# Performance work log

Hardware: AMD Instinct MI355X
Metric: run time of the kernel (lower is better)

The kernel has to match this reference:

```python
import jax, jax.numpy as jnp
import numpy as np

H_DIM = 2048
N_HEADS = 16
HEAD_DIM = H_DIM // N_HEADS
B, S = 2, 2048


def setup_inputs() -> dict:
    key = jax.random.key(0)
    ks = jax.random.split(key, 10)
    sc = 1.0 / np.sqrt(H_DIM)
    return {
        "X": jax.random.normal(ks[0], (B, S, H_DIM), dtype=jnp.float32),
        "attention_mask": jnp.ones((B, S, S), dtype=jnp.int32),
        "Wq": jax.random.normal(ks[1], (H_DIM, H_DIM), dtype=jnp.float32) * sc,
        "bq": jnp.zeros((H_DIM,), dtype=jnp.float32),
        "Wk": jax.random.normal(ks[2], (H_DIM, H_DIM), dtype=jnp.float32) * sc,
        "bk": jnp.zeros((H_DIM,), dtype=jnp.float32),
        "Wv": jax.random.normal(ks[3], (H_DIM, H_DIM), dtype=jnp.float32) * sc,
        "bv": jnp.zeros((H_DIM,), dtype=jnp.float32),
        "Wo": jax.random.normal(ks[4], (H_DIM, H_DIM), dtype=jnp.float32) * sc,
        "bo": jnp.zeros((H_DIM,), dtype=jnp.float32),
    }


def reference(X, attention_mask, Wq, bq, Wk, bk, Wv, bv, Wo, bo):
    b, s, _ = X.shape
    # QKV projections -> [b, heads, s, head_dim]
    def proj(W, bias):
        y = jnp.einsum("bsd,de->bse", X, W) + bias
        return y.reshape(b, s, N_HEADS, HEAD_DIM).transpose(0, 2, 1, 3)
    Q, K, V = proj(Wq, bq), proj(Wk, bk), proj(Wv, bv)
    # scores [b, h, s, s]
    scores = jnp.einsum("bhqd,bhkd->bhqk", Q, K) / jnp.sqrt(jnp.float32(HEAD_DIM))
    mask = attention_mask[:, None, :, :]  # [b,1,s,s]
    scores = jnp.where(mask == 0, jnp.float32(-jnp.inf), scores)
    attn = jax.nn.softmax(scores, axis=-1)
    # dropout_rate = 0.0 -> no-op
    out = jnp.einsum("bhqk,bhkd->bhqd", attn, V)
    out = out.transpose(0, 2, 1, 3).reshape(b, s, H_DIM)
    return jnp.einsum("bsd,de->bse", out, Wo) + bo
```

## Files before the change

### kernel.cpp

```cpp
#include <hip/hip_runtime.h>
#include <hip/hip_bf16.h>

#define H_DIM 2048
#define N_HEADS 16
#define HEAD_DIM 128
#define BATCH 2
#define SEQ 2048

typedef __bf16 bf16_t;
typedef __bf16 bf16x8 __attribute__((ext_vector_type(8)));
typedef float f32x4 __attribute__((ext_vector_type(4)));

#define MFMA16(a, b, c) __builtin_amdgcn_mfma_f32_16x16x32_bf16((a), (b), (c), 0, 0, 0)

#define GLOAD16(gp, lp) __builtin_amdgcn_global_load_lds( \
    (const __attribute__((address_space(1))) void*)(gp),  \
    (__attribute__((address_space(3))) void*)(lp), 16, 0, 0)

__global__ __launch_bounds__(256) void detect_kernel(const unsigned int* __restrict__ X,
                                                     int* __restrict__ flags) {
    __shared__ int cnt[256];
    int t = threadIdx.x;
    int c = 0;
    for (int i = 0; i < 16; i++) {
        unsigned w  = X[t * 16 + i];
        unsigned lo = w & 0xFFFFu;
        unsigned e  = (lo >> 7) & 0xFFu;
        if (lo == 0u || (e >= 100u && e <= 141u)) c++;
    }
    cnt[t] = c;
    __syncthreads();
    for (int s = 128; s > 0; s >>= 1) {
        if (t < s) cnt[t] += cnt[t + s];
        __syncthreads();
    }
    if (t == 0) { flags[0] = (cnt[0] >= 2048) ? 1 : 0; flags[1] = 1; }
}

__global__ __launch_bounds__(256) void maskcheck_kernel(const int* __restrict__ mask,
                                                        int* __restrict__ flags) {
    size_t i = ((size_t)blockIdx.x * 256 + threadIdx.x) * 8;
    const int4* p = (const int4*)(mask + i);
    int4 a = p[0], b = p[1];
    int all = (a.x != 0) & (a.y != 0) & (a.z != 0) & (a.w != 0) &
              (b.x != 0) & (b.y != 0) & (b.z != 0) & (b.w != 0);
    if (!all) atomicAnd(&flags[1], 0);
}

__device__ inline bf16x8 load8(const void* __restrict__ p, size_t idx, int isbf16) {
    if (isbf16) {
        return *(const bf16x8*)((const bf16_t*)p + idx);
    } else {
        const float* f = (const float*)p + idx;
        float4 a = *(const float4*)f;
        float4 b = *(const float4*)(f + 4);
        bf16x8 r;
        r[0] = (bf16_t)a.x; r[1] = (bf16_t)a.y; r[2] = (bf16_t)a.z; r[3] = (bf16_t)a.w;
        r[4] = (bf16_t)b.x; r[5] = (bf16_t)b.y; r[6] = (bf16_t)b.z; r[7] = (bf16_t)b.w;
        return r;
    }
}

__device__ inline float readf(const void* __restrict__ p, int idx, int isbf16) {
    return isbf16 ? (float)((const bf16_t*)p)[idx] : ((const float*)p)[idx];
}

__global__ __launch_bounds__(256) void convert_kernel(const void* __restrict__ X,
                                                      bf16_t* __restrict__ Xb,
                                                      const int* __restrict__ flags) {
    const int isbf16 = flags[0];
    size_t i = ((size_t)blockIdx.x * 256 + threadIdx.x) * 8;
    bf16x8 v = load8(X, i, isbf16);
    *(bf16x8*)(Xb + i) = v;
}

__global__ __launch_bounds__(256) void transpose_kernel(
    const void* __restrict__ W0, const void* __restrict__ W1,
    const void* __restrict__ W2, const void* __restrict__ W3,
    bf16_t* __restrict__ Wts, const int* __restrict__ flags)
{
    const int isbf16 = flags[0];
    const int z = blockIdx.z;
    const void* W = (z == 0) ? W0 : (z == 1) ? W1 : (z == 2) ? W2 : W3;
    bf16_t* out = Wts + (size_t)z * H_DIM * H_DIM;

    __shared__ __attribute__((aligned(16))) bf16_t Ts[64][72];
    const int tid = threadIdx.x;
    const int n0 = blockIdx.x * 64;
    const int k0 = blockIdx.y * 64;

    #pragma unroll
    for (int j = 0; j < 2; j++) {
        int idx = j * 2048 + tid * 8;
        int r = idx >> 6, c = idx & 63;
        bf16x8 v = load8(W, (size_t)(k0 + r) * H_DIM + n0 + c, isbf16);
        *(bf16x8*)(&Ts[r][c]) = v;
    }
    __syncthreads();
    const int wr = tid & 63;
    const int wcg = (tid >> 6) * 8;
    #pragma unroll
    for (int j = 0; j < 2; j++) {
        int wc = wcg + j * 32;
        bf16x8 o;
        #pragma unroll
        for (int u = 0; u < 8; u++) o[u] = Ts[wc + u][wr];
        *(bf16x8*)(&out[(size_t)(n0 + wr) * H_DIM + k0 + wc]) = o;
    }
}

__global__ __launch_bounds__(256) void gemm_qkv_kernel(
    const bf16_t* __restrict__ A, const bf16_t* __restrict__ Wts,
    const void* __restrict__ b0, const void* __restrict__ b1, const void* __restrict__ b2,
    bf16_t* __restrict__ qws, bf16_t* __restrict__ kws, bf16_t* __restrict__ vtws,
    const int* __restrict__ flags)
{
    const int isbf16 = flags[0];
    const int z = blockIdx.z;
    const bf16_t* Wt = Wts + (size_t)z * H_DIM * H_DIM;
    const void* bias = (z == 0) ? b0 : (z == 1) ? b1 : b2;
    bf16_t* dst = (z == 0) ? qws : (z == 1) ? kws : vtws;

    __shared__ __attribute__((aligned(16))) bf16_t As[4][128][8];
    __shared__ __attribute__((aligned(16))) bf16_t Bs[4][128][8];

    const int tid  = threadIdx.x;
    const int lane = tid & 63;
    const int wid  = tid >> 6;
    const int quad = lane >> 4;
    const int l16  = lane & 15;
    const int wm   = (wid >> 1) * 64;
    const int wn   = (wid & 1) * 64;
    const int m0   = blockIdx.y * 128;
    const int n0   = blockIdx.x * 128;

    f32x4 acc[4][4] = {};

    for (int k0 = 0; k0 < H_DIM; k0 += 32) {
        #pragma unroll
        for (int j = 0; j < 2; j++) {
            int slot = j * 256 + tid;
            int k8 = slot >> 7, row = slot & 127;
            GLOAD16(A  + (size_t)(m0 + row) * H_DIM + k0 + k8 * 8, (bf16_t*)As + slot * 8);
            GLOAD16(Wt + (size_t)(n0 + row) * H_DIM + k0 + k8 * 8, (bf16_t*)Bs + slot * 8);
        }
        __syncthreads();
        bf16x8 af[4], bfr[4];
        #pragma unroll
        for (int i = 0; i < 4; i++) {
            af[i]  = *(const bf16x8*)(&As[quad][wm + i * 16 + l16][0]);
            bfr[i] = *(const bf16x8*)(&Bs[quad][wn + i * 16 + l16][0]);
        }
        #pragma unroll
        for (int mi = 0; mi < 4; mi++)
            #pragma unroll
            for (int ni = 0; ni < 4; ni++)
                acc[mi][ni] = MFMA16(af[mi], bfr[ni], acc[mi][ni]);
        __syncthreads();
    }

    #pragma unroll
    for (int ni = 0; ni < 4; ni++) {
        int col = n0 + wn + ni * 16 + l16;
        int h = col >> 7, d = col & (HEAD_DIM - 1);
        float bv = readf(bias, col, isbf16);
        #pragma unroll
        for (int mi = 0; mi < 4; mi++) {
            int row0 = m0 + wm + mi * 16 + quad * 4;
            int b = row0 >> 11;
            if (z < 2) {
                #pragma unroll
                for (int r = 0; r < 4; r++) {
                    int s = (row0 + r) & (SEQ - 1);
                    dst[((size_t)(b * N_HEADS + h) * SEQ + s) * HEAD_DIM + d] =
                        (bf16_t)(acc[mi][ni][r] + bv);
                }
            } else {
                int s0 = row0 & (SEQ - 1);
                bf16_t o[4];
                #pragma unroll
                for (int r = 0; r < 4; r++) o[r] = (bf16_t)(acc[mi][ni][r] + bv);
                *(unsigned long long*)(&dst[((size_t)(b * N_HEADS + h) * HEAD_DIM + d) * SEQ + s0]) =
                    *(unsigned long long*)o;
            }
        }
    }
}

__global__ __launch_bounds__(256) void gemm_out_kernel(
    const bf16_t* __restrict__ A, const bf16_t* __restrict__ Wt,
    const void* __restrict__ bias, void* __restrict__ C,
    const int* __restrict__ flags)
{
    const int isbf16 = flags[0];
    __shared__ __attribute__((aligned(16))) bf16_t As[4][128][8];
    __shared__ __attribute__((aligned(16))) bf16_t Bs[4][128][8];

    const int tid  = threadIdx.x;
    const int lane = tid & 63;
    const int wid  = tid >> 6;
    const int quad = lane >> 4;
    const int l16  = lane & 15;
    const int wm   = (wid >> 1) * 64;
    const int wn   = (wid & 1) * 64;
    const int m0   = blockIdx.y * 128;
    const int n0   = blockIdx.x * 128;

    f32x4 acc[4][4] = {};

    for (int k0 = 0; k0 < H_DIM; k0 += 32) {
        #pragma unroll
        for (int j = 0; j < 2; j++) {
            int slot = j * 256 + tid;
            int k8 = slot >> 7, row = slot & 127;
            GLOAD16(A  + (size_t)(m0 + row) * H_DIM + k0 + k8 * 8, (bf16_t*)As + slot * 8);
            GLOAD16(Wt + (size_t)(n0 + row) * H_DIM + k0 + k8 * 8, (bf16_t*)Bs + slot * 8);
        }
        __syncthreads();
        bf16x8 af[4], bfr[4];
        #pragma unroll
        for (int i = 0; i < 4; i++) {
            af[i]  = *(const bf16x8*)(&As[quad][wm + i * 16 + l16][0]);
            bfr[i] = *(const bf16x8*)(&Bs[quad][wn + i * 16 + l16][0]);
        }
        #pragma unroll
        for (int mi = 0; mi < 4; mi++)
            #pragma unroll
            for (int ni = 0; ni < 4; ni++)
                acc[mi][ni] = MFMA16(af[mi], bfr[ni], acc[mi][ni]);
        __syncthreads();
    }

    #pragma unroll
    for (int ni = 0; ni < 4; ni++) {
        int col = n0 + wn + ni * 16 + l16;
        float bv = readf(bias, col, isbf16);
        #pragma unroll
        for (int mi = 0; mi < 4; mi++) {
            int row0 = m0 + wm + mi * 16 + quad * 4;
            #pragma unroll
            for (int r = 0; r < 4; r++) {
                float v = acc[mi][ni][r] + bv;
                if (isbf16) ((bf16_t*)C)[(size_t)(row0 + r) * H_DIM + col] = (bf16_t)v;
                else        ((float*)C)[(size_t)(row0 + r) * H_DIM + col]  = v;
            }
        }
    }
}

__global__ __launch_bounds__(256) void attn_kernel(
    const bf16_t* __restrict__ Q, const bf16_t* __restrict__ K,
    const bf16_t* __restrict__ Vt, const int* __restrict__ mask,
    const int* __restrict__ flags, bf16_t* __restrict__ ctx)
{
    __shared__ __attribute__((aligned(16))) bf16_t Ks[2][16][64][8];
    __shared__ __attribute__((aligned(16))) bf16_t Vs[2][8][128][8];
    __shared__ __attribute__((aligned(16))) bf16_t Pl[4][16][72];

    const int tid  = threadIdx.x;
    const int lane = tid & 63;
    const int wid  = tid >> 6;
    const int quad = lane >> 4;
    const int l16  = lane & 15;

    const int bh = blockIdx.y;
    const int b  = bh >> 4, h = bh & 15;
    const int q_base = blockIdx.x * 64 + wid * 16;
    const int maskAll = flags[1];

    const bf16_t* Qp = Q  + (size_t)bh * SEQ * HEAD_DIM;
    const bf16_t* Kp = K  + (size_t)bh * SEQ * HEAD_DIM;
    const bf16_t* Vp = Vt + (size_t)bh * HEAD_DIM * SEQ;
    const int*    mp = mask + (size_t)b * SEQ * SEQ;

    bf16x8 qf[4];
    #pragma unroll
    for (int t = 0; t < 4; t++)
        qf[t] = *(const bf16x8*)(Qp + (size_t)(q_base + l16) * HEAD_DIM + t * 32 + quad * 8);

    const float CS = 0.1275260013f;
    float m_r[4], l_r[4];
    #pragma unroll
    for (int r = 0; r < 4; r++) { m_r[r] = -1e30f; l_r[r] = 0.0f; }
    f32x4 o_acc[8] = {};

    auto stage = [&](int kt, int bb) {
        const int key0 = kt * 64;
        #pragma unroll
        for (int j = 0; j < 4; j++) {
            int slot = j * 256 + tid;
            int krow = slot & 63, k8 = slot >> 6;
            GLOAD16(Kp + (size_t)(key0 + krow) * HEAD_DIM + k8 * 8,
                    (bf16_t*)(&Ks[bb][0][0][0]) + slot * 8);
        }
        #pragma unroll
        for (int j = 0; j < 4; j++) {
            int slot = j * 256 + tid;
            int d = slot & 127, kq = slot >> 7;
            GLOAD16(Vp + (size_t)d * SEQ + key0 + kq * 8,
                    (bf16_t*)(&Vs[bb][0][0][0]) + slot * 8);
        }
    };

    stage(0, 0);

    const int NKT = SEQ / 64;
    for (int kt = 0; kt < NKT; kt++) {
        const int bb = kt & 1;
        const int key0 = kt * 64;
        __syncthreads();
        if (kt + 1 < NKT) stage(kt + 1, bb ^ 1);

        f32x4 s_acc[4];
        #pragma unroll
        for (int nt = 0; nt < 4; nt++) {
            f32x4 a = {};
            #pragma unroll
            for (int t = 0; t < 4; t++) {
                bf16x8 kf = *(const bf16x8*)(&Ks[bb][t * 4 + quad][nt * 16 + l16][0]);
                a = MFMA16(qf[t], kf, a);
            }
            s_acc[nt] = a;
        }

        float p2[4][4];
        #pragma unroll
        for (int nt = 0; nt < 4; nt++)
            #pragma unroll
            for (int r = 0; r < 4; r++)
                p2[nt][r] = s_acc[nt][r] * CS;

        if (!maskAll) {
            #pragma unroll
            for (int nt = 0; nt < 4; nt++) {
                int key = key0 + nt * 16 + l16;
                #pragma unroll
                for (int r = 0; r < 4; r++) {
                    int q = q_base + quad * 4 + r;
                    if (mp[(size_t)q * SEQ + key] == 0) p2[nt][r] = -1e30f;
                }
            }
        }

        #pragma unroll
        for (int r = 0; r < 4; r++) {
            float tmax = fmaxf(fmaxf(p2[0][r], p2[1][r]), fmaxf(p2[2][r], p2[3][r]));
            #pragma unroll
            for (int off = 1; off < 16; off <<= 1)
                tmax = fmaxf(tmax, __shfl_xor(tmax, off));
            float mnew  = fmaxf(m_r[r], tmax);
            float alpha = exp2f(m_r[r] - mnew);
            m_r[r] = mnew;
            float rsum = 0.0f;
            #pragma unroll
            for (int nt = 0; nt < 4; nt++) {
                float pv = exp2f(p2[nt][r] - mnew);
                p2[nt][r] = pv;
                rsum += pv;
            }
            #pragma unroll
            for (int off = 1; off < 16; off <<= 1)
                rsum += __shfl_xor(rsum, off);
            l_r[r] = l_r[r] * alpha + rsum;
            #pragma unroll
            for (int dn = 0; dn < 8; dn++)
                o_acc[dn][r] *= alpha;
        }

        #pragma unroll
        for (int nt = 0; nt < 4; nt++)
            #pragma unroll
            for (int r = 0; r < 4; r++)
                Pl[wid][quad * 4 + r][nt * 16 + l16] = (bf16_t)p2[nt][r];

        #pragma unroll
        for (int t = 0; t < 2; t++) {
            bf16x8 pf = *(const bf16x8*)(&Pl[wid][l16][t * 32 + quad * 8]);
            #pragma unroll
            for (int dn = 0; dn < 8; dn++) {
                bf16x8 vf = *(const bf16x8*)(&Vs[bb][t * 4 + quad][dn * 16 + l16][0]);
                o_acc[dn] = MFMA16(pf, vf, o_acc[dn]);
            }
        }
    }

    #pragma unroll
    for (int dn = 0; dn < 8; dn++) {
        #pragma unroll
        for (int r = 0; r < 4; r++) {
            int q = q_base + quad * 4 + r;
            int d = dn * 16 + l16;
            float v = o_acc[dn][r] / l_r[r];
            ctx[((size_t)(b * SEQ + q) * N_HEADS + h) * HEAD_DIM + d] = (bf16_t)v;
        }
    }
}

extern "C" void kernel_launch(void* const* d_in, const int* in_sizes, int n_in,
                              void* d_out, int out_size, void* d_ws, size_t ws_size,
                              hipStream_t stream) {
    const void* X    = d_in[0];
    const int*  mask = (const int*)d_in[1];
    const void* Wq   = d_in[2];
    const void* bq   = d_in[3];
    const void* Wk   = d_in[4];
    const void* bk   = d_in[5];
    const void* Wv   = d_in[6];
    const void* bv   = d_in[7];
    const void* Wo   = d_in[8];
    const void* bo   = d_in[9];

    const size_t NE = (size_t)BATCH * SEQ * H_DIM;
    const size_t NW = (size_t)H_DIM * H_DIM;

    int*    flags = (int*)d_ws;
    bf16_t* Xb    = (bf16_t*)((char*)d_ws + 256);
    bf16_t* Wts   = Xb + NE;
    bf16_t* qws   = Wts + 4 * NW;
    bf16_t* kws   = qws + NE;
    bf16_t* vtws  = kws + NE;
    bf16_t* cws   = vtws + NE;

    detect_kernel<<<1, 256, 0, stream>>>((const unsigned int*)X, flags);
    maskcheck_kernel<<<(BATCH * SEQ * SEQ) / (256 * 8), 256, 0, stream>>>(mask, flags);
    convert_kernel<<<NE / (256 * 8), 256, 0, stream>>>(X, Xb, flags);
    transpose_kernel<<<dim3(32, 32, 4), 256, 0, stream>>>(Wq, Wk, Wv, Wo, Wts, flags);
    gemm_qkv_kernel<<<dim3(H_DIM / 128, (BATCH * SEQ) / 128, 3), 256, 0, stream>>>(
        Xb, Wts, bq, bk, bv, qws, kws, vtws, flags);
    attn_kernel<<<dim3(SEQ / 64, BATCH * N_HEADS), 256, 0, stream>>>(
        qws, kws, vtws, mask, flags, cws);
    gemm_out_kernel<<<dim3(H_DIM / 128, (BATCH * SEQ) / 128), 256, 0, stream>>>(
        cws, Wts + 3 * NW, bo, d_out, flags);
}
```

Measured before the change: 701.3 us.

## Double-buffer LDS tiles in QKV and output projection GEMMs

Both projection GEMM kernels now use two LDS buffers per operand. The next K-slice is prefetched with global_load_lds right after the barrier, while MFMAs run on the current slice, and one of the two barriers per iteration is removed. The aim is to hide global-load latency behind matrix compute. In exchange, LDS use per block doubles, which may reduce occupancy, and the kernels rely on the barrier's wait covering the outstanding async LDS loads.

New measurement: 709.5 us. About the same (+1.2%).

```diff
diff --git a/kernel.cpp b/kernel.cpp
--- a/kernel.cpp
+++ b/kernel.cpp
@@ -121,8 +121,8 @@
     const void* bias = (z == 0) ? b0 : (z == 1) ? b1 : b2;
     bf16_t* dst = (z == 0) ? qws : (z == 1) ? kws : vtws;
 
-    __shared__ __attribute__((aligned(16))) bf16_t As[4][128][8];
-    __shared__ __attribute__((aligned(16))) bf16_t Bs[4][128][8];
+    __shared__ __attribute__((aligned(16))) bf16_t As[2][4][128][8];
+    __shared__ __attribute__((aligned(16))) bf16_t Bs[2][4][128][8];
 
     const int tid  = threadIdx.x;
     const int lane = tid & 63;
@@ -134,29 +134,41 @@
     const int m0   = blockIdx.y * 128;
     const int n0   = blockIdx.x * 128;
 
+    const int s_k8  = (tid * 2) >> 7;
+    const int s_row = (tid * 2) & 127;
+
     f32x4 acc[4][4] = {};
 
-    for (int k0 = 0; k0 < H_DIM; k0 += 32) {
+    auto stage = [&](int k0, int bb) {
         #pragma unroll
         for (int j = 0; j < 2; j++) {
             int slot = j * 256 + tid;
             int k8 = slot >> 7, row = slot & 127;
-            GLOAD16(A  + (size_t)(m0 + row) * H_DIM + k0 + k8 * 8, (bf16_t*)As + slot * 8);
-            GLOAD16(Wt + (size_t)(n0 + row) * H_DIM + k0 + k8 * 8, (bf16_t*)Bs + slot * 8);
-        }
+            GLOAD16(A  + (size_t)(m0 + row) * H_DIM + k0 + k8 * 8,
+                    (bf16_t*)(&As[bb][0][0][0]) + slot * 8);
+            GLOAD16(Wt + (size_t)(n0 + row) * H_DIM + k0 + k8 * 8,
+                    (bf16_t*)(&Bs[bb][0][0][0]) + slot * 8);
+        }
+    };
+
+    stage(0, 0);
+    const int NIT = H_DIM / 32;
+    for (int it = 0; it < NIT; it++) {
+        const int bb = it & 1;
         __syncthreads();
+        if (it + 1 < NIT) stage((it + 1) * 32, bb ^ 1);
+
         bf16x8 af[4], bfr[4];
         #pragma unroll
         for (int i = 0; i < 4; i++) {
-            af[i]  = *(const bf16x8*)(&As[quad][wm + i * 16 + l16][0]);
-            bfr[i] = *(const bf16x8*)(&Bs[quad][wn + i * 16 + l16][0]);
+            af[i]  = *(const bf16x8*)(&As[bb][quad][wm + i * 16 + l16][0]);
+            bfr[i] = *(const bf16x8*)(&Bs[bb][quad][wn + i * 16 + l16][0]);
         }
         #pragma unroll
         for (int mi = 0; mi < 4; mi++)
             #pragma unroll
             for (int ni = 0; ni < 4; ni++)
                 acc[mi][ni] = MFMA16(af[mi], bfr[ni], acc[mi][ni]);
-        __syncthreads();
     }
 
     #pragma unroll
@@ -193,8 +205,8 @@
     const int* __restrict__ flags)
 {
     const int isbf16 = flags[0];
-    __shared__ __attribute__((aligned(16))) bf16_t As[4][128][8];
-    __shared__ __attribute__((aligned(16))) bf16_t Bs[4][128][8];
+    __shared__ __attribute__((aligned(16))) bf16_t As[2][4][128][8];
+    __shared__ __attribute__((aligned(16))) bf16_t Bs[2][4][128][8];
 
     const int tid  = threadIdx.x;
     const int lane = tid & 63;
@@ -208,27 +220,36 @@
 
     f32x4 acc[4][4] = {};
 
-    for (int k0 = 0; k0 < H_DIM; k0 += 32) {
+    auto stage = [&](int k0, int bb) {
         #pragma unroll
         for (int j = 0; j < 2; j++) {
             int slot = j * 256 + tid;
             int k8 = slot >> 7, row = slot & 127;
-            GLOAD16(A  + (size_t)(m0 + row) * H_DIM + k0 + k8 * 8, (bf16_t*)As + slot * 8);
-            GLOAD16(Wt + (size_t)(n0 + row) * H_DIM + k0 + k8 * 8, (bf16_t*)Bs + slot * 8);
-        }
+            GLOAD16(A  + (size_t)(m0 + row) * H_DIM + k0 + k8 * 8,
+                    (bf16_t*)(&As[bb][0][0][0]) + slot * 8);
+            GLOAD16(Wt + (size_t)(n0 + row) * H_DIM + k0 + k8 * 8,
+                    (bf16_t*)(&Bs[bb][0][0][0]) + slot * 8);
+        }
+    };
+
+    stage(0, 0);
+    const int NIT = H_DIM / 32;
+    for (int it = 0; it < NIT; it++) {
+        const int bb = it & 1;
         __syncthreads();
+        if (it + 1 < NIT) stage((it + 1) * 32, bb ^ 1);
+
         bf16x8 af[4], bfr[4];
         #pragma unroll
         for (int i = 0; i < 4; i++) {
-            af[i]  = *(const bf16x8*)(&As[quad][wm + i * 16 + l16][0]);
-            bfr[i] = *(const bf16x8*)(&Bs[quad][wn + i * 16 + l16][0]);
+            af[i]  = *(const bf16x8*)(&As[bb][quad][wm + i * 16 + l16][0]);
+            bfr[i] = *(const bf16x8*)(&Bs[bb][quad][wn + i * 16 + l16][0]);
         }
         #pragma unroll
         for (int mi = 0; mi < 4; mi++)
             #pragma unroll
             for (int ni = 0; ni < 4; ni++)
                 acc[mi][ni] = MFMA16(af[mi], bfr[ni], acc[mi][ni]);
-        __syncthreads();
     }
 
     #pragma unroll
```
